# Optimization experiments

Hardware: AMD Instinct MI355X
Metric: run time of the kernel (lower is better)

Reference implementation:

```python
import jax, jax.numpy as jnp
import numpy as np

B, T, N = 16, 2048, 24
K, C_IN, C0, C1 = 3, 1, 64, 64
KS, PRED_LEN = 3, 24
EPS = 1e-5


def _norm_laplacian(adj):
    # L = D^-1/2 A^T D^-1/2 (matches scipy path: (A D^-1/2)^T D^-1/2)
    d = adj.sum(axis=1)
    dis = jnp.where(d > 0, 1.0 / jnp.sqrt(d), 0.0)
    return dis[:, None] * adj.T * dis[None, :]


def _cheb_stack(L, k_terms):
    polys = [jnp.eye(N, dtype=L.dtype), L]
    for _ in range(2, k_terms):
        polys.append(2.0 * L @ polys[-1] - polys[-2])
    return jnp.stack(polys[:k_terms])  # (K, N, N)


def _causal_conv(x, w, b, dilation):
    ks = w.shape[-1]
    pad = (ks - 1) * dilation
    x = jnp.pad(x, ((0, 0), (0, 0), (0, 0), (pad, 0)))
    y = jax.lax.conv_general_dilated(
        x, w, window_strides=(1, 1), padding='VALID',
        rhs_dilation=(1, dilation),
        dimension_numbers=('NCHW', 'OIHW', 'NCHW'))
    return y + b[None, :, None, None]


def _bn(x, g, be):
    # training-mode batch norm over (B, N, T) per channel
    mu = x.mean(axis=(0, 2, 3), keepdims=True)
    var = x.var(axis=(0, 2, 3), keepdims=True)
    return g[None, :, None, None] * (x - mu) * jax.lax.rsqrt(var + EPS) + be[None, :, None, None]


def setup_inputs() -> dict:
    key = jax.random.key(0)
    ks = jax.random.split(key, 16)
    s = 0.05
    return {
        'batch_x': jax.random.normal(ks[0], (B, T, N), jnp.float32),
        'adj': jax.random.uniform(ks[1], (N, N), jnp.float32),
        'theta': jax.random.normal(ks[2], (K, C_IN, C0), jnp.float32),  # Theta per Cheb term
        'w1a': jax.random.normal(ks[3], (C0, C0, 1, KS), jnp.float32) * s,
        'b1a': jnp.zeros((C0,), jnp.float32),
        'g1a': jnp.ones((C0,), jnp.float32), 'be1a': jnp.zeros((C0,), jnp.float32),
        'w1b': jax.random.normal(ks[4], (C0, C0, 1, KS), jnp.float32) * s,
        'b1b': jnp.zeros((C0,), jnp.float32),
        'g1b': jnp.ones((C0,), jnp.float32), 'be1b': jnp.zeros((C0,), jnp.float32),
        'w2a': jax.random.normal(ks[5], (C1, C0, 1, KS), jnp.float32) * s,
        'b2a': jnp.zeros((C1,), jnp.float32),
        'g2a': jnp.ones((C1,), jnp.float32), 'be2a': jnp.zeros((C1,), jnp.float32),
        'w2b': jax.random.normal(ks[6], (C1, C1, 1, KS), jnp.float32) * s,
        'b2b': jnp.zeros((C1,), jnp.float32),
        'g2b': jnp.ones((C1,), jnp.float32), 'be2b': jnp.zeros((C1,), jnp.float32),
        'w_end': jax.random.normal(ks[7], (C1 // 2, C1, 1, 1), jnp.float32) * s,
        'b_end': jnp.zeros((C1 // 2,), jnp.float32),
        'w_end1': jax.random.normal(ks[8], (1, C1 // 2, 1, 2), jnp.float32) * s,
        'b_end1': jnp.zeros((1,), jnp.float32),
    }


def reference(batch_x, adj, theta,
              w1a, b1a, g1a, be1a, w1b, b1b, g1b, be1b,
              w2a, b2a, g2a, be2a, w2b, b2b, g2b, be2b,
              w_end, b_end, w_end1, b_end1):
    # (B, T, N) -> (B, 1, N, T)
    x = jnp.transpose(batch_x, (0, 2, 1))[:, None, :, :]

    # --- Cheb_conv: fused over K terms and all timesteps ---
    L = _norm_laplacian(adj)
    Tk = _cheb_stack(L, K)                       # (K, N, N)
    xp = jnp.transpose(x, (0, 2, 1, 3))          # (B, N, C_in, T)
    # out[b,o,n,t] = sum_{k,m,c} xp[b,m,c,t] Tk[k,m,n] theta[k,c,o]
    gc = jnp.einsum('bmct,kmn,kco->bont', xp, Tk, theta)  # (B, C0, N, T)

    # --- TCN block 1 (dilation 1), residual is identity (C0 == C0) ---
    h = jax.nn.relu(_bn(_causal_conv(gc, w1a, b1a, 1), g1a, be1a))
    h = jax.nn.relu(_bn(_causal_conv(h, w1b, b1b, 1), g1b, be1b))
    out0 = jax.nn.relu(h + gc)

    # --- TCN block 2 (dilation 2), residual identity (C0 == C1), no final relu ---
    h = jax.nn.relu(_bn(_causal_conv(out0, w2a, b2a, 2), g2a, be2a))
    h = jax.nn.relu(_bn(_causal_conv(h, w2b, b2b, 2), g2b, be2b))
    out = h + out0                               # (B, C1, N, T)

    # --- head: 1x1 conv + relu, then (1,2) valid conv -> 1 channel ---
    e = jax.lax.conv_general_dilated(out, w_end, (1, 1), 'VALID',
                                     dimension_numbers=('NCHW', 'OIHW', 'NCHW'))
    e = jax.nn.relu(e + b_end[None, :, None, None])
    e = jax.lax.conv_general_dilated(e, w_end1, (1, 1), 'VALID',
                                     dimension_numbers=('NCHW', 'OIHW', 'NCHW'))
    e = e + b_end1[None, :, None, None]          # (B, 1, N, T-1)
    e = e[:, 0, :, -PRED_LEN:]                   # (B, N, pred_len)
    return jnp.transpose(e, (0, 2, 1))           # (B, pred_len, N)
```

## Files before the change

### kernel.cpp

```cpp
#include <hip/hip_runtime.h>
#include <cmath>

#define TPB 256

typedef __attribute__((ext_vector_type(8)))  short short8;
typedef __attribute__((ext_vector_type(16))) float float16;

static constexpr int  BB   = 16;
static constexpr int  TDIM = 2048;
static constexpr int  NN   = 24;
static constexpr int  P    = BB * NN;
static constexpr int  C    = 64;
static constexpr int  TILE = 256;
static constexpr int  NBT  = TDIM / TILE;
static constexpr int  NSHARD = 64;
static constexpr float INV_CNT = 1.0f / 786432.0f;
static constexpr int  XPITCH = 72;

static constexpr size_t OFF_TK    = 0;
static constexpr size_t OFF_WEFF  = 6912;
static constexpr size_t OFF_WFRAG = 9216;
static constexpr size_t OFF_ST    = 82944;
static constexpr size_t OFF_O0    = 216320;
static constexpr size_t OFF_YT    = 2673920;
static constexpr size_t OFF_S     = 5131520;
static constexpr size_t OFF_YA    = 14568704;
static constexpr size_t OFF_YB    = 115232000;

__device__ __forceinline__ unsigned short f2bf(float f) {
    unsigned int i = __float_as_uint(f);
    i += 0x7FFFu + ((i >> 16) & 1u);
    return (unsigned short)(i >> 16);
}
__device__ __forceinline__ float bf2f(unsigned short u) {
    return __uint_as_float((unsigned)u << 16);
}
__device__ __forceinline__ unsigned pk2bf(float a, float b) {
    unsigned ua = __float_as_uint(a) + 0x8000u;
    unsigned ub = __float_as_uint(b) + 0x8000u;
    return __builtin_amdgcn_perm(ub, ua, 0x07060302u);
}

__device__ __forceinline__
void bn_from_stats(const float* __restrict__ statsIn, const float* __restrict__ g,
                   const float* __restrict__ be, float2* abl, int tid)
{
    const int ch = tid >> 2, q = tid & 3;
    float s1 = 0.f, s2 = 0.f;
    #pragma unroll
    for (int u = 0; u < 4; ++u) {
        float4 a = *(const float4*)(statsIn + tid * 16 + u * 4);
        float4 b = *(const float4*)(statsIn + 4096 + tid * 16 + u * 4);
        s1 += a.x + a.y + a.z + a.w;
        s2 += b.x + b.y + b.z + b.w;
    }
    s1 += __shfl_xor(s1, 1); s1 += __shfl_xor(s1, 2);
    s2 += __shfl_xor(s2, 1); s2 += __shfl_xor(s2, 2);
    if (q == 0) {
        float mu  = s1 * INV_CNT;
        float var = s2 * INV_CNT - mu * mu;
        float a = g[ch] * (1.0f / sqrtf(var + 1e-5f));
        abl[ch] = make_float2(a, be[ch] - mu * a);
    }
}

__global__ __launch_bounds__(TPB)
void prep_kernel(const float* __restrict__ adj, const float* __restrict__ theta,
                 const float* __restrict__ w1a,
                 const float* __restrict__ w1b, const float* __restrict__ w2a,
                 const float* __restrict__ w2b,
                 float* __restrict__ tk, float* __restrict__ weff,
                 unsigned short* __restrict__ wf, float* __restrict__ stats)
{
    const int tid = threadIdx.x;
    if (blockIdx.x < 144) {
        int e = blockIdx.x * TPB + tid;
        int conv = e / 12288, r = e % 12288;
        int oh = r / 6144; r %= 6144;
        int kc = r / 512;  r %= 512;
        int lane = r / 8;
        int jj = r % 8;
        int o = oh * 32 + (lane & 31);
        int K = kc * 16 + (lane >> 5) * 8 + jj;
        int j = K / 64, c2 = K % 64;
        const float* w = (conv == 0) ? w1b : ((conv == 1) ? w2a : w2b);
        wf[e] = f2bf(w[(o * 64 + c2) * 3 + j]);
        return;
    }

    __shared__ float disl[24];
    __shared__ float Ll[576];
    __shared__ float T2l[576];

    for (int e = tid; e < 4 * 8192; e += TPB) stats[e] = 0.f;

    if (tid < 24) {
        float d = 0.f;
        for (int j = 0; j < 24; ++j) d += adj[tid * 24 + j];
        disl[tid] = (d > 0.f) ? 1.0f / sqrtf(d) : 0.f;
    }
    __syncthreads();
    for (int e = tid; e < 576; e += TPB) {
        int i = e / 24, j = e % 24;
        Ll[e] = disl[i] * adj[j * 24 + i] * disl[j];
    }
    __syncthreads();
    for (int e = tid; e < 576; e += TPB) {
        int i = e / 24, j = e % 24;
        float a = 0.f;
        for (int m = 0; m < 24; ++m) a += Ll[i * 24 + m] * Ll[m * 24 + j];
        T2l[e] = 2.f * a - ((i == j) ? 1.f : 0.f);
    }
    __syncthreads();
    for (int e = tid; e < 576; e += TPB) {
        int i = e / 24, j = e % 24;
        tk[e]        = (i == j) ? 1.f : 0.f;
        tk[576 + e]  = Ll[e];
        tk[1152 + e] = T2l[e];
    }
    for (int e = tid; e < 576; e += TPB) {
        int o = e / 9, k = (e % 9) / 3, j = e % 3;
        float a = 0.f;
        for (int c2 = 0; c2 < 64; ++c2)
            a += w1a[(o * 64 + c2) * 3 + j] * theta[k * 64 + c2];
        weff[(k * 3 + j) * 64 + o] = a;
    }
}

__global__ __launch_bounds__(TPB)
void s_kernel(const float* __restrict__ bx, const float* __restrict__ tk,
              float* __restrict__ sbuf)
{
    __shared__ float bxs[256 * 25];
    __shared__ float tkl[576];
    const int tid = threadIdx.x;
    const int blk = blockIdx.x;
    const int b  = blk / 24;
    const int r  = blk % 24;
    const int k  = r >> 3;
    const int t0 = (r & 7) * 256;

    for (int e = tid; e < 576; e += TPB) tkl[e] = tk[k * 576 + e];
    for (int e = tid; e < 256 * 24; e += TPB) {
        int t = e / 24, m = e % 24;
        bxs[t * 25 + m] = bx[((long)b * TDIM + t0 + t) * NN + m];
    }
    __syncthreads();

    const int t = tid;
    float acc[24];
    #pragma unroll
    for (int n = 0; n < 24; ++n) acc[n] = 0.f;
    for (int m = 0; m < 24; ++m) {
        float xb = bxs[t * 25 + m];
        const float* tr = tkl + m * 24;
        #pragma unroll
        for (int n = 0; n < 24; ++n) acc[n] = fmaf(xb, tr[n], acc[n]);
    }
    for (int n = 0; n < 24; ++n)
        sbuf[((long)k * P + b * NN + n) * TDIM + t0 + t] = acc[n];
}

__global__ __launch_bounds__(TPB)
void stats1a_kernel(const float* __restrict__ sbuf, const float* __restrict__ weff,
                    float* __restrict__ statsOut)
{
    __shared__ float4 ssl4[3 * 66];
    __shared__ float4 wl4[144];
    __shared__ float  part[4][2][64];
    const int tid = threadIdx.x;
    const int blk = blockIdx.x;
    const int p  = blk >> 3;
    const int t0 = (blk & 7) * 256;

    for (int e = tid; e < 576; e += TPB) ((float*)wl4)[e] = weff[e];
    for (int e = tid; e < 3 * 65; e += TPB) {
        int k = e / 65, u4 = e % 65;
        int t = t0 - 4 + u4 * 4;
        float4 v = make_float4(0.f, 0.f, 0.f, 0.f);
        if (t >= 0) v = *(const float4*)(sbuf + ((long)k * P + p) * TDIM + t);
        ssl4[k * 66 + u4] = v;
    }
    __syncthreads();

    const int oq = tid & 7;
    const int tq = tid >> 3;
    float acc[8][8];
    #pragma unroll
    for (int i = 0; i < 8; ++i)
        #pragma unroll
        for (int ti = 0; ti < 8; ++ti) acc[i][ti] = 0.f;

    #pragma unroll
    for (int k = 0; k < 3; ++k) {
        float4 x0 = ssl4[k * 66 + tq * 2];
        float4 x1 = ssl4[k * 66 + tq * 2 + 1];
        float4 x2 = ssl4[k * 66 + tq * 2 + 2];
        float xv[12] = { x0.x,x0.y,x0.z,x0.w, x1.x,x1.y,x1.z,x1.w, x2.x,x2.y,x2.z,x2.w };
        #pragma unroll
        for (int j = 0; j < 3; ++j) {
            float4 w0 = wl4[(k * 3 + j) * 16 + oq * 2];
            float4 w1 = wl4[(k * 3 + j) * 16 + oq * 2 + 1];
            float wv[8] = { w0.x,w0.y,w0.z,w0.w, w1.x,w1.y,w1.z,w1.w };
            #pragma unroll
            for (int i = 0; i < 8; ++i)
                #pragma unroll
                for (int ti = 0; ti < 8; ++ti)
                    acc[i][ti] = fmaf(wv[i], xv[ti + 2 + j], acc[i][ti]);
        }
    }

    float s1v[8], s2v[8];
    #pragma unroll
    for (int i = 0; i < 8; ++i) {
        float a1 = 0.f, a2 = 0.f;
        #pragma unroll
        for (int ti = 0; ti < 8; ++ti) { a1 += acc[i][ti]; a2 += acc[i][ti] * acc[i][ti]; }
        s1v[i] = a1; s2v[i] = a2;
    }
    #pragma unroll
    for (int m = 8; m < 64; m <<= 1) {
        #pragma unroll
        for (int i = 0; i < 8; ++i) {
            s1v[i] += __shfl_xor(s1v[i], m);
            s2v[i] += __shfl_xor(s2v[i], m);
        }
    }
    const int wave = tid >> 6, lane = tid & 63;
    if (lane < 8) {
        #pragma unroll
        for (int i = 0; i < 8; ++i) {
            part[wave][0][oq * 8 + i] = s1v[i];
            part[wave][1][oq * 8 + i] = s2v[i];
        }
    }
    __syncthreads();
    if (tid < 128) {
        int s = tid >> 6, o = tid & 63;
        float tot = part[0][s][o] + part[1][s][o] + part[2][s][o] + part[3][s][o];
        atomicAdd(&statsOut[(s * 64 + o) * NSHARD + (blk & 63)], tot);
    }
}

template<int MODE>
__global__ __launch_bounds__(TPB)
void conv_mfma(const float* __restrict__ sbuf, const unsigned short* __restrict__ yin,
               unsigned short* __restrict__ yout, float* __restrict__ ytail,
               const unsigned short* __restrict__ wf, const float* __restrict__ weff,
               const float* __restrict__ statsIn, const float* __restrict__ g,
               const float* __restrict__ be, float* __restrict__ statsOut,
               const float* __restrict__ theta, float* __restrict__ o0s)
{
    __shared__ unsigned short Xl[260 * XPITCH];
    __shared__ float  ssl[(MODE <= 1) ? 3 * 264 : 4];
    __shared__ float  weffl[(MODE == 0) ? 576 : 4];
    __shared__ float  thl[(MODE == 1) ? 192 : 4];
    __shared__ float2 abl[64];
    __shared__ float  parts[(MODE <= 1) ? 4 * 8 * 8 * 2 : 4 * 2 * 16 * 2];

    const int tid  = threadIdx.x;
    const int lane = tid & 63;
    const int w    = tid >> 6;
    const int oh   = w & 1;
    const int l31  = lane & 31;
    const int h    = lane >> 5;
    const int blk  = blockIdx.x;
    const int p    = blk >> 3;
    const int tile = blk & 7;
    const int t0   = tile * TILE;

    short8 af[12];
    #pragma unroll
    for (int kc = 0; kc < 12; ++kc)
        af[kc] = *((const short8*)wf + (oh * 12 + kc) * 64 + lane);

    bn_from_stats(statsIn, g, be, abl, tid);

    if (MODE == 0)
        for (int e = tid; e < 576; e += TPB) weffl[e] = weff[e];
    if (MODE == 1)
        for (int e = tid; e < 192; e += TPB) thl[e] = theta[e];
    if (MODE <= 1) {
        for (int e = tid; e < 3 * 66; e += TPB) {
            int k = e / 66, u4 = e % 66;
            int t = t0 - 8 + u4 * 4;
            float4 v = make_float4(0.f, 0.f, 0.f, 0.f);
            if (t >= 0) v = *(const float4*)(sbuf + ((long)k * P + p) * TDIM + t);
            *(float4*)(ssl + k * 264 + u4 * 4) = v;
        }
    }
    __syncthreads();

    const unsigned short* yinb = (MODE >= 1)
        ? (yin + ((long)p * TDIM + t0 - 4) * 64) : nullptr;
    for (int e = tid; e < 260 * 8; e += TPB) {
        const int tt = e >> 3, cb = e & 7;
        const int t = t0 - 4 + tt;
        float xv[8];
        if (t < 0) {
            #pragma unroll
            for (int r = 0; r < 8; ++r) xv[r] = 0.f;
        } else if (MODE == 0) {
            float sv[9];
            #pragma unroll
            for (int k = 0; k < 3; ++k)
                #pragma unroll
                for (int j = 0; j < 3; ++j)
                    sv[k * 3 + j] = ssl[k * 264 + tt + 2 + j];
            #pragma unroll
            for (int r = 0; r < 8; ++r) {
                int c = cb * 8 + r;
                float raw = 0.f;
                #pragma unroll
                for (int q = 0; q < 9; ++q)
                    raw = fmaf(weffl[q * 64 + c], sv[q], raw);
                float2 ab = abl[c];
                xv[r] = fmaxf(fmaf(ab.x, raw, ab.y), 0.f);
            }
        } else {
            short8 yv8 = *(const short8*)(yinb + (long)e * 8);
            float gcb[3];
            if (MODE == 1) {
                gcb[0] = ssl[      tt + 4];
                gcb[1] = ssl[264 + tt + 4];
                gcb[2] = ssl[528 + tt + 4];
            }
            #pragma unroll
            for (int r = 0; r < 8; ++r) {
                int c = cb * 8 + r;
                float2 ab = abl[c];
                float v = bf2f((unsigned short)yv8[r]);
                float hh = fmaxf(fmaf(ab.x, v, ab.y), 0.f);
                if (MODE == 1) {
                    float gc = thl[c] * gcb[0] + thl[64 + c] * gcb[1] + thl[128 + c] * gcb[2];
                    hh = fmaxf(hh + gc, 0.f);
                }
                xv[r] = hh;
            }
        }
        if (MODE == 1 && tile == 7 && tt >= 235) {
            #pragma unroll
            for (int r = 0; r < 8; ++r)
                o0s[(long)p * 1600 + (cb * 8 + r) * 25 + (tt - 235)] = xv[r];
        }
        uint4 pk;
        pk.x = pk2bf(xv[0], xv[1]);
        pk.y = pk2bf(xv[2], xv[3]);
        pk.z = pk2bf(xv[4], xv[5]);
        pk.w = pk2bf(xv[6], xv[7]);
        *(uint4*)(Xl + tt * XPITCH + cb * 8) = pk;
    }
    __syncthreads();

    float16 acc[4];
    #pragma unroll
    for (int i = 0; i < 4; ++i)
        #pragma unroll
        for (int r = 0; r < 16; ++r) acc[i][r] = 0.f;

    const int tqb = (w >> 1) * 4;
    #pragma unroll
    for (int kc = 0; kc < 12; ++kc) {
        const int j = kc >> 2;
        const int roff = (MODE == 0) ? (2 + j) : (2 * j);
        const int cbase = (kc & 3) * 16 + h * 8;
        #pragma unroll
        for (int i = 0; i < 4; ++i) {
            int row = (tqb + i) * 32 + l31 + roff;
            short8 bfr = *(const short8*)(Xl + row * XPITCH + cbase);
            acc[i] = __builtin_amdgcn_mfma_f32_32x32x16_bf16(af[kc], bfr, acc[i], 0, 0, 0);
        }
    }

    if (MODE <= 1) {
        __syncthreads();

        #pragma unroll
        for (int i = 0; i < 4; ++i) {
            int tl = (tqb + i) * 32 + l31;
            #pragma unroll
            for (int q = 0; q < 4; ++q) {
                int ob = oh * 32 + 8 * q + 4 * h;
                uint2 pk;
                pk.x = pk2bf(acc[i][4 * q + 0], acc[i][4 * q + 1]);
                pk.y = pk2bf(acc[i][4 * q + 2], acc[i][4 * q + 3]);
                *(uint2*)(Xl + tl * XPITCH + ob) = pk;
            }
        }
        __syncthreads();

        const int cb = tid & 7;
        unsigned short* youtb = yout + ((long)p * TDIM + t0) * 64;
        float s1[8], s2[8];
        #pragma unroll
        for (int r = 0; r < 8; ++r) { s1[r] = 0.f; s2[r] = 0.f; }
        for (int e = tid; e < 2048; e += TPB) {
            int tt = e >> 3;
            uint4 v = *(const uint4*)(Xl + tt * XPITCH + cb * 8);
            *(uint4*)(youtb + (long)e * 8) = v;
            unsigned uu[4] = { v.x, v.y, v.z, v.w };
            #pragma unroll
            for (int q = 0; q < 4; ++q) {
                float f0 = __uint_as_float(uu[q] << 16);
                float f1 = __uint_as_float(uu[q] & 0xFFFF0000u);
                s1[2 * q]     += f0;  s2[2 * q]     = fmaf(f0, f0, s2[2 * q]);
                s1[2 * q + 1] += f1;  s2[2 * q + 1] = fmaf(f1, f1, s2[2 * q + 1]);
            }
        }
        #pragma unroll
        for (int m = 8; m <= 32; m <<= 1) {
            #pragma unroll
            for (int r = 0; r < 8; ++r) {
                s1[r] += __shfl_xor(s1[r], m);
                s2[r] += __shfl_xor(s2[r], m);
            }
        }
        if (lane < 8) {
            #pragma unroll
            for (int r = 0; r < 8; ++r) {
                parts[((w * 8 + lane) * 8 + r) * 2 + 0] = s1[r];
                parts[((w * 8 + lane) * 8 + r) * 2 + 1] = s2[r];
            }
        }
        __syncthreads();
        if (tid < 64) {
            int o = tid, cbo = o >> 3, r = o & 7;
            float t1 = 0.f, t2 = 0.f;
            #pragma unroll
            for (int ww = 0; ww < 4; ++ww) {
                t1 += parts[((ww * 8 + cbo) * 8 + r) * 2 + 0];
                t2 += parts[((ww * 8 + cbo) * 8 + r) * 2 + 1];
            }
            atomicAdd(&statsOut[o * NSHARD + (blk & 63)], t1);
            atomicAdd(&statsOut[(64 + o) * NSHARD + (blk & 63)], t2);
        }
    } else {
        if (tile == 7) {
            #pragma unroll
            for (int i = 0; i < 4; ++i) {
                int tg = t0 + (tqb + i) * 32 + l31;
                if (tg >= TDIM - 25) {
                    #pragma unroll
                    for (int r = 0; r < 16; ++r) {
                        int o = oh * 32 + (r & 3) + 8 * (r >> 2) + 4 * h;
                        ytail[((long)p * C + o) * 25 + (tg - (TDIM - 25))] = acc[i][r];
                    }
                }
            }
        }
        float s1[16], s2[16];
        #pragma unroll
        for (int r = 0; r < 16; ++r) {
            float a1 = 0.f, a2 = 0.f;
            #pragma unroll
            for (int i = 0; i < 4; ++i) { float v = acc[i][r]; a1 += v; a2 = fmaf(v, v, a2); }
            s1[r] = a1; s2[r] = a2;
        }
        #pragma unroll
        for (int m = 1; m <= 16; m <<= 1) {
            #pragma unroll
            for (int r = 0; r < 16; ++r) {
                s1[r] += __shfl_xor(s1[r], m);
                s2[r] += __shfl_xor(s2[r], m);
            }
        }
        if (l31 == 0) {
            #pragma unroll
            for (int r = 0; r < 16; ++r) {
                parts[(((w * 2 + h) * 16) + r) * 2 + 0] = s1[r];
                parts[(((w * 2 + h) * 16) + r) * 2 + 1] = s2[r];
            }
        }
        __syncthreads();
        if (tid < 64) {
            int o = tid;
            int ohh = o >> 5, v = o & 31;
            int hh = (v >> 2) & 1, r = (v & 3) + 4 * (v >> 3);
            float t1 = parts[(((ohh * 2 + hh) * 16) + r) * 2 + 0]
                     + parts[((((ohh + 2) * 2 + hh) * 16) + r) * 2 + 0];
            float t2 = parts[(((ohh * 2 + hh) * 16) + r) * 2 + 1]
                     + parts[((((ohh + 2) * 2 + hh) * 16) + r) * 2 + 1];
            atomicAdd(&statsOut[o * NSHARD + (blk & 63)], t1);
            atomicAdd(&statsOut[(64 + o) * NSHARD + (blk & 63)], t2);
        }
    }
}

__global__ __launch_bounds__(TPB)
void end_kernel(const float* __restrict__ ytail, const float* __restrict__ o0s,
                const float* __restrict__ statsIn, const float* __restrict__ g,
                const float* __restrict__ be, const float* __restrict__ w_end,
                const float* __restrict__ b_end, const float* __restrict__ w_end1,
                const float* __restrict__ b_end1, float* __restrict__ out)
{
    __shared__ float2 abl[64];
    __shared__ float outl[64 * 25];
    __shared__ float e1l[32 * 25];
    __shared__ float wendl[2048];
    const int tid = threadIdx.x;
    const int p = blockIdx.x;
    const int b = p / 24, n = p % 24;

    bn_from_stats(statsIn, g, be, abl, tid);
    for (int e = tid; e < 2048; e += TPB) wendl[e] = w_end[e];
    __syncthreads();

    for (int e = tid; e < 1600; e += TPB) {
        int c = e / 25, tau = e % 25;
        float v = ytail[((long)p * C + c) * 25 + tau];
        float2 ab = abl[c];
        outl[e] = fmaxf(ab.x * v + ab.y, 0.f) + o0s[(long)p * 1600 + e];
    }
    __syncthreads();
    for (int e = tid; e < 800; e += TPB) {
        int q = e / 25, tau = e % 25;
        float a = b_end[q];
        for (int c = 0; c < 64; ++c)
            a = fmaf(wendl[q * 64 + c], outl[c * 25 + tau], a);
        e1l[e] = fmaxf(a, 0.f);
    }
    __syncthreads();
    if (tid < 24) {
        float a = b_end1[0];
        #pragma unroll
        for (int q = 0; q < 32; ++q)
            a += w_end1[q * 2] * e1l[q * 25 + tid] + w_end1[q * 2 + 1] * e1l[q * 25 + tid + 1];
        out[((long)b * 24 + tid) * 24 + n] = a;
    }
}

extern "C" void kernel_launch(void* const* d_in, const int* in_sizes, int n_in,
                              void* d_out, int out_size, void* d_ws, size_t ws_size,
                              hipStream_t stream)
{
    (void)in_sizes; (void)n_in; (void)out_size; (void)ws_size;
    const float* bx    = (const float*)d_in[0];
    const float* adj   = (const float*)d_in[1];
    const float* theta = (const float*)d_in[2];
    const float* w1a   = (const float*)d_in[3];
    const float* g1a   = (const float*)d_in[5];
    const float* be1a  = (const float*)d_in[6];
    const float* w1b   = (const float*)d_in[7];
    const float* g1b   = (const float*)d_in[9];
    const float* be1b  = (const float*)d_in[10];
    const float* w2a   = (const float*)d_in[11];
    const float* g2a   = (const float*)d_in[13];
    const float* be2a  = (const float*)d_in[14];
    const float* w2b   = (const float*)d_in[15];
    const float* g2b   = (const float*)d_in[17];
    const float* be2b  = (const float*)d_in[18];
    const float* wend  = (const float*)d_in[19];
    const float* bend  = (const float*)d_in[20];
    const float* wend1 = (const float*)d_in[21];
    const float* bend1 = (const float*)d_in[22];

    char* ws = (char*)d_ws;
    float*          tk    = (float*)(ws + OFF_TK);
    float*          weff  = (float*)(ws + OFF_WEFF);
    unsigned short* wf    = (unsigned short*)(ws + OFF_WFRAG);
    float*          stats = (float*)(ws + OFF_ST);
    float*          o0s   = (float*)(ws + OFF_O0);
    float*          ytail = (float*)(ws + OFF_YT);
    float*          sb    = (float*)(ws + OFF_S);
    unsigned short* yA    = (unsigned short*)(ws + OFF_YA);
    unsigned short* yB    = (unsigned short*)(ws + OFF_YB);

    prep_kernel   <<<145, TPB, 0, stream>>>(adj, theta, w1a, w1b, w2a, w2b,
                                            tk, weff, wf, stats);
    s_kernel      <<<384, TPB, 0, stream>>>(bx, tk, sb);
    stats1a_kernel<<<P * NBT, TPB, 0, stream>>>(sb, weff, stats);

    conv_mfma<0><<<P * NBT, TPB, 0, stream>>>(
        sb, nullptr, yA, nullptr, wf, weff,
        stats, g1a, be1a, stats + 8192, nullptr, nullptr);
    conv_mfma<1><<<P * NBT, TPB, 0, stream>>>(
        sb, yA, yB, nullptr, wf + 12288, nullptr,
        stats + 8192, g1b, be1b, stats + 16384, theta, o0s);
    conv_mfma<2><<<P * NBT, TPB, 0, stream>>>(
        sb, yB, nullptr, ytail, wf + 24576, nullptr,
        stats + 16384, g2a, be2a, stats + 24576, nullptr, nullptr);

    end_kernel<<<P, TPB, 0, stream>>>(ytail, o0s, stats + 24576, g2b, be2b,
                                      wend, bend, wend1, bend1, (float*)d_out);
}
```

Before: 363.1 us.

## Process two nodes per conv block to amortize weight/BN setup and batch loads

Each conv_mfma block now handles two (batch,node) rows, one after the other, so the grid is halved. The weight fragments, BN coefficients and small tables are loaded once and reused for both rows. The per-row input loads are unrolled into a register batch of 9 short8 loads issued before any conversion, which exposes memory-level parallelism. This costs more shared memory for the source staging buffer, fewer blocks in flight, and extra serialization between the two rows through the added syncs.

Result: slower. 447.1 us (+23.1%).

```diff
diff --git a/kernel.cpp b/kernel.cpp
--- a/kernel.cpp
+++ b/kernel.cpp
@@ -10,6 +10,7 @@
 static constexpr int  TDIM = 2048;
 static constexpr int  NN   = 24;
 static constexpr int  P    = BB * NN;
+static constexpr int  HP   = P / 2;
 static constexpr int  C    = 64;
 static constexpr int  TILE = 256;
 static constexpr int  NBT  = TDIM / TILE;
@@ -252,11 +253,11 @@
                const float* __restrict__ theta, float* __restrict__ o0s)
 {
     __shared__ unsigned short Xl[260 * XPITCH];
-    __shared__ float  ssl[(MODE <= 1) ? 3 * 264 : 4];
+    __shared__ float  ssl[(MODE <= 1) ? 2 * 3 * 264 : 4];
     __shared__ float  weffl[(MODE == 0) ? 576 : 4];
     __shared__ float  thl[(MODE == 1) ? 192 : 4];
     __shared__ float2 abl[64];
-    __shared__ float  parts[(MODE <= 1) ? 4 * 8 * 8 * 2 : 4 * 2 * 16 * 2];
+    __shared__ float  parts[(MODE <= 1) ? 512 : 256];
 
     const int tid  = threadIdx.x;
     const int lane = tid & 63;
@@ -265,7 +266,7 @@
     const int l31  = lane & 31;
     const int h    = lane >> 5;
     const int blk  = blockIdx.x;
-    const int p    = blk >> 3;
+    const int pair = blk >> 3;
     const int tile = blk & 7;
     const int t0   = tile * TILE;
 
@@ -276,212 +277,237 @@
 
     bn_from_stats(statsIn, g, be, abl, tid);
 
-    if (MODE == 0)
-        for (int e = tid; e < 576; e += TPB) weffl[e] = weff[e];
-    if (MODE == 1)
-        for (int e = tid; e < 192; e += TPB) thl[e] = theta[e];
+    if (MODE == 0) {
+        #pragma unroll
+        for (int it = 0; it < 3; ++it) {
+            int e = tid + it * 256;
+            if (e < 576) weffl[e] = weff[e];
+        }
+    }
+    if (MODE == 1) {
+        if (tid < 192) thl[tid] = theta[tid];
+    }
     if (MODE <= 1) {
-        for (int e = tid; e < 3 * 66; e += TPB) {
-            int k = e / 66, u4 = e % 66;
-            int t = t0 - 8 + u4 * 4;
-            float4 v = make_float4(0.f, 0.f, 0.f, 0.f);
-            if (t >= 0) v = *(const float4*)(sbuf + ((long)k * P + p) * TDIM + t);
-            *(float4*)(ssl + k * 264 + u4 * 4) = v;
-        }
-    }
-    __syncthreads();
-
-    const unsigned short* yinb = (MODE >= 1)
-        ? (yin + ((long)p * TDIM + t0 - 4) * 64) : nullptr;
-    for (int e = tid; e < 260 * 8; e += TPB) {
-        const int tt = e >> 3, cb = e & 7;
-        const int t = t0 - 4 + tt;
-        float xv[8];
-        if (t < 0) {
-            #pragma unroll
-            for (int r = 0; r < 8; ++r) xv[r] = 0.f;
-        } else if (MODE == 0) {
-            float sv[9];
-            #pragma unroll
-            for (int k = 0; k < 3; ++k)
-                #pragma unroll
-                for (int j = 0; j < 3; ++j)
-                    sv[k * 3 + j] = ssl[k * 264 + tt + 2 + j];
-            #pragma unroll
-            for (int r = 0; r < 8; ++r) {
-                int c = cb * 8 + r;
-                float raw = 0.f;
-                #pragma unroll
-                for (int q = 0; q < 9; ++q)
-                    raw = fmaf(weffl[q * 64 + c], sv[q], raw);
-                float2 ab = abl[c];
-                xv[r] = fmaxf(fmaf(ab.x, raw, ab.y), 0.f);
+        #pragma unroll
+        for (int it = 0; it < 2; ++it) {
+            int e = tid + it * 256;
+            if (e < 396) {
+                int q = e / 198, rr = e % 198;
+                int k = rr / 66, u4 = rr % 66;
+                int t = t0 - 8 + u4 * 4;
+                int pq = pair + q * HP;
+                float4 v = make_float4(0.f, 0.f, 0.f, 0.f);
+                if (t >= 0) v = *(const float4*)(sbuf + ((long)k * P + pq) * TDIM + t);
+                *(float4*)(ssl + q * 792 + k * 264 + u4 * 4) = v;
+            }
+        }
+    }
+
+    for (int q = 0; q < 2; ++q) {
+        const int pp = pair + q * HP;
+        __syncthreads();
+
+        short8 yv[9];
+        if (MODE >= 1) {
+            const unsigned short* yinb = yin + ((long)pp * TDIM + t0 - 4) * 64;
+            #pragma unroll
+            for (int it = 0; it < 9; ++it) {
+                int e = tid + it * 256;
+                int ec = (e < 2080) ? e : 2079;
+                yv[it] = *(const short8*)(yinb + (long)ec * 8);
+            }
+        }
+
+        #pragma unroll
+        for (int it = 0; it < 9; ++it) {
+            const int e = tid + it * 256;
+            if (e >= 2080) break;
+            const int tt = e >> 3, cb = e & 7;
+            const int t = t0 - 4 + tt;
+            float xv[8];
+            if (t < 0) {
+                #pragma unroll
+                for (int r = 0; r < 8; ++r) xv[r] = 0.f;
+            } else if (MODE == 0) {
+                float sv[9];
+                #pragma unroll
+                for (int k = 0; k < 3; ++k)
+                    #pragma unroll
+                    for (int j = 0; j < 3; ++j)
+                        sv[k * 3 + j] = ssl[q * 792 + k * 264 + tt + 2 + j];
+                #pragma unroll
+                for (int r = 0; r < 8; ++r) {
+                    int c = cb * 8 + r;
+                    float raw = 0.f;
+                    #pragma unroll
+                    for (int u = 0; u < 9; ++u)
+                        raw = fmaf(weffl[u * 64 + c], sv[u], raw);
+                    float2 ab = abl[c];
+                    xv[r] = fmaxf(fmaf(ab.x, raw, ab.y), 0.f);
+                }
+            } else {
+                float gcb[3];
+                if (MODE == 1) {
+                    gcb[0] = ssl[q * 792 +       tt + 4];
+                    gcb[1] = ssl[q * 792 + 264 + tt + 4];
+                    gcb[2] = ssl[q * 792 + 528 + tt + 4];
+                }
+                #pragma unroll
+                for (int r = 0; r < 8; ++r) {
+                    int c = cb * 8 + r;
+                    float2 ab = abl[c];
+                    float v = bf2f((unsigned short)yv[it][r]);
+                    float hh = fmaxf(fmaf(ab.x, v, ab.y), 0.f);
+                    if (MODE == 1) {
+                        float gc = thl[c] * gcb[0] + thl[64 + c] * gcb[1] + thl[128 + c] * gcb[2];
+                        hh = fmaxf(hh + gc, 0.f);
+                    }
+                    xv[r] = hh;
+                }
+            }
+            if (MODE == 1 && tile == 7 && tt >= 235) {
+                #pragma unroll
+                for (int r = 0; r < 8; ++r)
+                    o0s[(long)pp * 1600 + (cb * 8 + r) * 25 + (tt - 235)] = xv[r];
+            }
+            uint4 pk;
+            pk.x = pk2bf(xv[0], xv[1]);
+            pk.y = pk2bf(xv[2], xv[3]);
+            pk.z = pk2bf(xv[4], xv[5]);
+            pk.w = pk2bf(xv[6], xv[7]);
+            *(uint4*)(Xl + tt * XPITCH + cb * 8) = pk;
+        }
+        __syncthreads();
+
+        float16 acc[4];
+        #pragma unroll
+        for (int i = 0; i < 4; ++i)
+            #pragma unroll
+            for (int r = 0; r < 16; ++r) acc[i][r] = 0.f;
+
+        const int tqb = (w >> 1) * 4;
+        #pragma unroll
+        for (int kc = 0; kc < 12; ++kc) {
+            const int j = kc >> 2;
+            const int roff = (MODE == 0) ? (2 + j) : (2 * j);
+            const int cbase = (kc & 3) * 16 + h * 8;
+            #pragma unroll
+            for (int i = 0; i < 4; ++i) {
+                int row = (tqb + i) * 32 + l31 + roff;
+                short8 bfr = *(const short8*)(Xl + row * XPITCH + cbase);
+                acc[i] = __builtin_amdgcn_mfma_f32_32x32x16_bf16(af[kc], bfr, acc[i], 0, 0, 0);
+            }
+        }
+
+        if (MODE <= 1) {
+            __syncthreads();
+
+            #pragma unroll
+            for (int i = 0; i < 4; ++i) {
+                int tl = (tqb + i) * 32 + l31;
+                #pragma unroll
+                for (int qq = 0; qq < 4; ++qq) {
+                    int ob = oh * 32 + 8 * qq + 4 * h;
+                    uint2 pk;
+                    pk.x = pk2bf(acc[i][4 * qq + 0], acc[i][4 * qq + 1]);
+                    pk.y = pk2bf(acc[i][4 * qq + 2], acc[i][4 * qq + 3]);
+                    *(uint2*)(Xl + tl * XPITCH + ob) = pk;
+                }
+            }
+            __syncthreads();
+
+            const int cb = tid & 7;
+            unsigned short* youtb = yout + ((long)pp * TDIM + t0) * 64;
+            float s1[8], s2[8];
+            #pragma unroll
+            for (int r = 0; r < 8; ++r) { s1[r] = 0.f; s2[r] = 0.f; }
+            #pragma unroll
+            for (int it = 0; it < 8; ++it) {
+                int e = tid + it * 256;
+                int tt = e >> 3;
+                uint4 v = *(const uint4*)(Xl + tt * XPITCH + cb * 8);
+                *(uint4*)(youtb + (long)e * 8) = v;
+                unsigned uu[4] = { v.x, v.y, v.z, v.w };
+                #pragma unroll
+                for (int qq = 0; qq < 4; ++qq) {
+                    float f0 = __uint_as_float(uu[qq] << 16);
+                    float f1 = __uint_as_float(uu[qq] & 0xFFFF0000u);
+                    s1[2 * qq]     += f0;  s2[2 * qq]     = fmaf(f0, f0, s2[2 * qq]);
+                    s1[2 * qq + 1] += f1;  s2[2 * qq + 1] = fmaf(f1, f1, s2[2 * qq + 1]);
+                }
+            }
+            #pragma unroll
+            for (int m = 8; m <= 32; m <<= 1) {
+                #pragma unroll
+                for (int r = 0; r < 8; ++r) {
+                    s1[r] += __shfl_xor(s1[r], m);
+                    s2[r] += __shfl_xor(s2[r], m);
+                }
+            }
+            if (lane < 8) {
+                float* pw = parts + (w * 8 + lane) * 16;
+                #pragma unroll
+                for (int r = 0; r < 8; ++r) { pw[r * 2] = s1[r]; pw[r * 2 + 1] = s2[r]; }
+            }
+            __syncthreads();
+            if (tid < 64) {
+                int o = tid, cbo = o >> 3, r = o & 7;
+                float t1 = 0.f, t2 = 0.f;
+                #pragma unroll
+                for (int ww = 0; ww < 4; ++ww) {
+                    t1 += parts[(ww * 8 + cbo) * 16 + r * 2];
+                    t2 += parts[(ww * 8 + cbo) * 16 + r * 2 + 1];
+                }
+                atomicAdd(&statsOut[o * NSHARD + (blk & 63)], t1);
+                atomicAdd(&statsOut[(64 + o) * NSHARD + (blk & 63)], t2);
             }
         } else {
-            short8 yv8 = *(const short8*)(yinb + (long)e * 8);
-            float gcb[3];
-            if (MODE == 1) {
-                gcb[0] = ssl[      tt + 4];
-                gcb[1] = ssl[264 + tt + 4];
-                gcb[2] = ssl[528 + tt + 4];
-            }
-            #pragma unroll
-            for (int r = 0; r < 8; ++r) {
-                int c = cb * 8 + r;
-                float2 ab = abl[c];
-                float v = bf2f((unsigned short)yv8[r]);
-                float hh = fmaxf(fmaf(ab.x, v, ab.y), 0.f);
-                if (MODE == 1) {
-                    float gc = thl[c] * gcb[0] + thl[64 + c] * gcb[1] + thl[128 + c] * gcb[2];
-                    hh = fmaxf(hh + gc, 0.f);
-                }
-                xv[r] = hh;
-            }
-        }
-        if (MODE == 1 && tile == 7 && tt >= 235) {
-            #pragma unroll
-            for (int r = 0; r < 8; ++r)
-                o0s[(long)p * 1600 + (cb * 8 + r) * 25 + (tt - 235)] = xv[r];
-        }
-        uint4 pk;
-        pk.x = pk2bf(xv[0], xv[1]);
-        pk.y = pk2bf(xv[2], xv[3]);
-        pk.z = pk2bf(xv[4], xv[5]);
-        pk.w = pk2bf(xv[6], xv[7]);
-        *(uint4*)(Xl + tt * XPITCH + cb * 8) = pk;
-    }
-    __syncthreads();
-
-    float16 acc[4];
-    #pragma unroll
-    for (int i = 0; i < 4; ++i)
-        #pragma unroll
-        for (int r = 0; r < 16; ++r) acc[i][r] = 0.f;
-
-    const int tqb = (w >> 1) * 4;
-    #pragma unroll
-    for (int kc = 0; kc < 12; ++kc) {
-        const int j = kc >> 2;
-        const int roff = (MODE == 0) ? (2 + j) : (2 * j);
-        const int cbase = (kc & 3) * 16 + h * 8;
-        #pragma unroll
-        for (int i = 0; i < 4; ++i) {
-            int row = (tqb + i) * 32 + l31 + roff;
-            short8 bfr = *(const short8*)(Xl + row * XPITCH + cbase);
-            acc[i] = __builtin_amdgcn_mfma_f32_32x32x16_bf16(af[kc], bfr, acc[i], 0, 0, 0);
-        }
-    }
-
-    if (MODE <= 1) {
-        __syncthreads();
-
-        #pragma unroll
-        for (int i = 0; i < 4; ++i) {
-            int tl = (tqb + i) * 32 + l31;
-            #pragma unroll
-            for (int q = 0; q < 4; ++q) {
-                int ob = oh * 32 + 8 * q + 4 * h;
-                uint2 pk;
-                pk.x = pk2bf(acc[i][4 * q + 0], acc[i][4 * q + 1]);
-                pk.y = pk2bf(acc[i][4 * q + 2], acc[i][4 * q + 3]);
-                *(uint2*)(Xl + tl * XPITCH + ob) = pk;
-            }
-        }
-        __syncthreads();
-
-        const int cb = tid & 7;
-        unsigned short* youtb = yout + ((long)p * TDIM + t0) * 64;
-        float s1[8], s2[8];
-        #pragma unroll
-        for (int r = 0; r < 8; ++r) { s1[r] = 0.f; s2[r] = 0.f; }
-        for (int e = tid; e < 2048; e += TPB) {
-            int tt = e >> 3;
-            uint4 v = *(const uint4*)(Xl + tt * XPITCH + cb * 8);
-            *(uint4*)(youtb + (long)e * 8) = v;
-            unsigned uu[4] = { v.x, v.y, v.z, v.w };
-            #pragma unroll
-            for (int q = 0; q < 4; ++q) {
-                float f0 = __uint_as_float(uu[q] << 16);
-                float f1 = __uint_as_float(uu[q] & 0xFFFF0000u);
-                s1[2 * q]     += f0;  s2[2 * q]     = fmaf(f0, f0, s2[2 * q]);
-                s1[2 * q + 1] += f1;  s2[2 * q + 1] = fmaf(f1, f1, s2[2 * q + 1]);
-            }
-        }
-        #pragma unroll
-        for (int m = 8; m <= 32; m <<= 1) {
-            #pragma unroll
-            for (int r = 0; r < 8; ++r) {
-                s1[r] += __shfl_xor(s1[r], m);
-                s2[r] += __shfl_xor(s2[r], m);
-            }
-        }
-        if (lane < 8) {
-            #pragma unroll
-            for (int r = 0; r < 8; ++r) {
-                parts[((w * 8 + lane) * 8 + r) * 2 + 0] = s1[r];
-                parts[((w * 8 + lane) * 8 + r) * 2 + 1] = s2[r];
-            }
-        }
-        __syncthreads();
-        if (tid < 64) {
-            int o = tid, cbo = o >> 3, r = o & 7;
-            float t1 = 0.f, t2 = 0.f;
-            #pragma unroll
-            for (int ww = 0; ww < 4; ++ww) {
-                t1 += parts[((ww * 8 + cbo) * 8 + r) * 2 + 0];
-                t2 += parts[((ww * 8 + cbo) * 8 + r) * 2 + 1];
-            }
-            atomicAdd(&statsOut[o * NSHARD + (blk & 63)], t1);
-            atomicAdd(&statsOut[(64 + o) * NSHARD + (blk & 63)], t2);
-        }
-    } else {
-        if (tile == 7) {
-            #pragma unroll
-            for (int i = 0; i < 4; ++i) {
-                int tg = t0 + (tqb + i) * 32 + l31;
-                if (tg >= TDIM - 25) {
-                    #pragma unroll
-                    for (int r = 0; r < 16; ++r) {
-                        int o = oh * 32 + (r & 3) + 8 * (r >> 2) + 4 * h;
-                        ytail[((long)p * C + o) * 25 + (tg - (TDIM - 25))] = acc[i][r];
+            if (tile == 7) {
+                #pragma unroll
+                for (int i = 0; i < 4; ++i) {
+                    int tg = t0 + (tqb + i) * 32 + l31;
+                    if (tg >= TDIM - 25) {
+                        #pragma unroll
+                        for (int r = 0; r < 16; ++r) {
+                            int o = oh * 32 + (r & 3) + 8 * (r >> 2) + 4 * h;
+                            ytail[((long)pp * C + o) * 25 + (tg - (TDIM - 25))] = acc[i][r];
+                        }
                     }
                 }
             }
-        }
-        float s1[16], s2[16];
-        #pragma unroll
-        for (int r = 0; r < 16; ++r) {
-            float a1 = 0.f, a2 = 0.f;
-            #pragma unroll
-            for (int i = 0; i < 4; ++i) { float v = acc[i][r]; a1 += v; a2 = fmaf(v, v, a2); }
-            s1[r] = a1; s2[r] = a2;
-        }
-        #pragma unroll
-        for (int m = 1; m <= 16; m <<= 1) {
+            float s1[16], s2[16];
             #pragma unroll
             for (int r = 0; r < 16; ++r) {
-                s1[r] += __shfl_xor(s1[r], m);
-                s2[r] += __shfl_xor(s2[r], m);
-            }
-        }
-        if (l31 == 0) {
-            #pragma unroll
-            for (int r = 0; r < 16; ++r) {
-                parts[(((w * 2 + h) * 16) + r) * 2 + 0] = s1[r];
-                parts[(((w * 2 + h) * 16) + r) * 2 + 1] = s2[r];
-            }
-        }
-        __syncthreads();
-        if (tid < 64) {
-            int o = tid;
-            int ohh = o >> 5, v = o & 31;
-            int hh = (v >> 2) & 1, r = (v & 3) + 4 * (v >> 3);
-            float t1 = parts[(((ohh * 2 + hh) * 16) + r) * 2 + 0]
-                     + parts[((((ohh + 2) * 2 + hh) * 16) + r) * 2 + 0];
-            float t2 = parts[(((ohh * 2 + hh) * 16) + r) * 2 + 1]
-                     + parts[((((ohh + 2) * 2 + hh) * 16) + r) * 2 + 1];
-            atomicAdd(&statsOut[o * NSHARD + (blk & 63)], t1);
-            atomicAdd(&statsOut[(64 + o) * NSHARD + (blk & 63)], t2);
+                float a1 = 0.f, a2 = 0.f;
+                #pragma unroll
+                for (int i = 0; i < 4; ++i) { float v = acc[i][r]; a1 += v; a2 = fmaf(v, v, a2); }
+                s1[r] = a1; s2[r] = a2;
+            }
+            #pragma unroll
+            for (int m = 1; m <= 16; m <<= 1) {
+                #pragma unroll
+                for (int r = 0; r < 16; ++r) {
+                    s1[r] += __shfl_xor(s1[r], m);
+                    s2[r] += __shfl_xor(s2[r], m);
+                }
+            }
+            if (l31 == 0) {
+                float* pw = parts + (w * 2 + h) * 32;
+                #pragma unroll
+                for (int r = 0; r < 16; ++r) { pw[r * 2] = s1[r]; pw[r * 2 + 1] = s2[r]; }
+            }
+            __syncthreads();
+            if (tid < 64) {
+                int o = tid;
+                int ohh = o >> 5, v = o & 31;
+                int hh = (v >> 2) & 1, r = (v & 3) + 4 * (v >> 3);
+                float t1 = parts[(ohh * 2 + hh) * 32 + r * 2]
+                         + parts[((ohh + 2) * 2 + hh) * 32 + r * 2];
+                float t2 = parts[(ohh * 2 + hh) * 32 + r * 2 + 1]
+                         + parts[((ohh + 2) * 2 + hh) * 32 + r * 2 + 1];
+                atomicAdd(&statsOut[o * NSHARD + (blk & 63)], t1);
+                atomicAdd(&statsOut[(64 + o) * NSHARD + (blk & 63)], t2);
+            }
         }
     }
 }
@@ -570,13 +596,13 @@
     s_kernel      <<<384, TPB, 0, stream>>>(bx, tk, sb);
     stats1a_kernel<<<P * NBT, TPB, 0, stream>>>(sb, weff, stats);
 
-    conv_mfma<0><<<P * NBT, TPB, 0, stream>>>(
+    conv_mfma<0><<<HP * NBT, TPB, 0, stream>>>(
         sb, nullptr, yA, nullptr, wf, weff,
         stats, g1a, be1a, stats + 8192, nullptr, nullptr);
-    conv_mfma<1><<<P * NBT, TPB, 0, stream>>>(
+    conv_mfma<1><<<HP * NBT, TPB, 0, stream>>>(
         sb, yA, yB, nullptr, wf + 12288, nullptr,
         stats + 8192, g1b, be1b, stats + 16384, theta, o0s);
-    conv_mfma<2><<<P * NBT, TPB, 0, stream>>>(
+    conv_mfma<2><<<HP * NBT, TPB, 0, stream>>>(
         sb, yB, nullptr, ytail, wf + 24576, nullptr,
         stats + 16384, g2a, be2a, stats + 24576, nullptr, nullptr);
 
```

## Precompute BN affine in tiny kernels, swizzle LDS tile, shrink shared memory

Applied to the files above, without the earlier changes.

Moves batch-norm stat reduction out of every conv block into single-block bnprep kernels, so each conv block just loads 64 precomputed scale/shift pairs. Replaces the padded LDS pitch with an XOR-swizzled 64-wide layout and aliases the scratch buffers, cutting shared memory per block. Adds launch_bounds occupancy hint of 4 blocks. Risks extra launch overhead from the four additional kernels.

After: 334.3 us. -7.9%, faster.

```diff
diff --git a/kernel.cpp b/kernel.cpp
--- a/kernel.cpp
+++ b/kernel.cpp
@@ -15,12 +15,12 @@
 static constexpr int  NBT  = TDIM / TILE;
 static constexpr int  NSHARD = 64;
 static constexpr float INV_CNT = 1.0f / 786432.0f;
-static constexpr int  XPITCH = 72;
 
 static constexpr size_t OFF_TK    = 0;
 static constexpr size_t OFF_WEFF  = 6912;
 static constexpr size_t OFF_WFRAG = 9216;
 static constexpr size_t OFF_ST    = 82944;
+static constexpr size_t OFF_BNAB  = 214016;
 static constexpr size_t OFF_O0    = 216320;
 static constexpr size_t OFF_YT    = 2673920;
 static constexpr size_t OFF_S     = 5131520;
@@ -40,28 +40,8 @@
     unsigned ub = __float_as_uint(b) + 0x8000u;
     return __builtin_amdgcn_perm(ub, ua, 0x07060302u);
 }
-
-__device__ __forceinline__
-void bn_from_stats(const float* __restrict__ statsIn, const float* __restrict__ g,
-                   const float* __restrict__ be, float2* abl, int tid)
-{
-    const int ch = tid >> 2, q = tid & 3;
-    float s1 = 0.f, s2 = 0.f;
-    #pragma unroll
-    for (int u = 0; u < 4; ++u) {
-        float4 a = *(const float4*)(statsIn + tid * 16 + u * 4);
-        float4 b = *(const float4*)(statsIn + 4096 + tid * 16 + u * 4);
-        s1 += a.x + a.y + a.z + a.w;
-        s2 += b.x + b.y + b.z + b.w;
-    }
-    s1 += __shfl_xor(s1, 1); s1 += __shfl_xor(s1, 2);
-    s2 += __shfl_xor(s2, 1); s2 += __shfl_xor(s2, 2);
-    if (q == 0) {
-        float mu  = s1 * INV_CNT;
-        float var = s2 * INV_CNT - mu * mu;
-        float a = g[ch] * (1.0f / sqrtf(var + 1e-5f));
-        abl[ch] = make_float2(a, be[ch] - mu * a);
-    }
+__device__ __forceinline__ int xidx(int tt, int ci) {
+    return tt * 64 + (((ci ^ (tt & 7)) << 3));
 }
 
 __global__ __launch_bounds__(TPB)
@@ -128,6 +108,29 @@
 }
 
 __global__ __launch_bounds__(TPB)
+void bnprep_kernel(const float* __restrict__ stats, const float* __restrict__ g,
+                   const float* __restrict__ be, float2* __restrict__ ab)
+{
+    const int tid = threadIdx.x;
+    const int ch = tid >> 2, q = tid & 3;
+    float s1 = 0.f, s2 = 0.f;
+    #pragma unroll
+    for (int u = 0; u < 16; ++u) {
+        int sh = q * 16 + u;
+        s1 += stats[ch * 64 + sh];
+        s2 += stats[(64 + ch) * 64 + sh];
+    }
+    s1 += __shfl_xor(s1, 1); s1 += __shfl_xor(s1, 2);
+    s2 += __shfl_xor(s2, 1); s2 += __shfl_xor(s2, 2);
+    if (q == 0) {
+        float mu  = s1 * INV_CNT;
+        float var = s2 * INV_CNT - mu * mu;
+        float a = g[ch] * (1.0f / sqrtf(var + 1e-5f));
+        ab[ch] = make_float2(a, be[ch] - mu * a);
+    }
+}
+
+__global__ __launch_bounds__(TPB)
 void s_kernel(const float* __restrict__ bx, const float* __restrict__ tk,
               float* __restrict__ sbuf)
 {
@@ -243,20 +246,22 @@
 }
 
 template<int MODE>
-__global__ __launch_bounds__(TPB)
+__global__ __launch_bounds__(TPB, 4)
 void conv_mfma(const float* __restrict__ sbuf, const unsigned short* __restrict__ yin,
                unsigned short* __restrict__ yout, float* __restrict__ ytail,
                const unsigned short* __restrict__ wf, const float* __restrict__ weff,
-               const float* __restrict__ statsIn, const float* __restrict__ g,
-               const float* __restrict__ be, float* __restrict__ statsOut,
+               const float2* __restrict__ bnab, float* __restrict__ statsOut,
                const float* __restrict__ theta, float* __restrict__ o0s)
 {
-    __shared__ unsigned short Xl[260 * XPITCH];
-    __shared__ float  ssl[(MODE <= 1) ? 3 * 264 : 4];
-    __shared__ float  weffl[(MODE == 0) ? 576 : 4];
-    __shared__ float  thl[(MODE == 1) ? 192 : 4];
+    constexpr int SCR = (MODE == 0) ? (792 + 576) : ((MODE == 1) ? (792 + 192) : 512);
+    __shared__ unsigned short Xl[260 * 64];
+    __shared__ float  scratch[SCR];
     __shared__ float2 abl[64];
-    __shared__ float  parts[(MODE <= 1) ? 4 * 8 * 8 * 2 : 4 * 2 * 16 * 2];
+
+    float* const ssl   = scratch;
+    float* const weffl = scratch + 792;
+    float* const thl   = scratch + 792;
+    float* const parts = scratch;
 
     const int tid  = threadIdx.x;
     const int lane = tid & 63;
@@ -274,12 +279,11 @@
     for (int kc = 0; kc < 12; ++kc)
         af[kc] = *((const short8*)wf + (oh * 12 + kc) * 64 + lane);
 
-    bn_from_stats(statsIn, g, be, abl, tid);
-
+    if (tid < 64) abl[tid] = bnab[tid];
     if (MODE == 0)
         for (int e = tid; e < 576; e += TPB) weffl[e] = weff[e];
     if (MODE == 1)
-        for (int e = tid; e < 192; e += TPB) thl[e] = theta[e];
+        if (tid < 192) thl[tid] = theta[tid];
     if (MODE <= 1) {
         for (int e = tid; e < 3 * 66; e += TPB) {
             int k = e / 66, u4 = e % 66;
@@ -312,8 +316,8 @@
                 int c = cb * 8 + r;
                 float raw = 0.f;
                 #pragma unroll
-                for (int q = 0; q < 9; ++q)
-                    raw = fmaf(weffl[q * 64 + c], sv[q], raw);
+                for (int u = 0; u < 9; ++u)
+                    raw = fmaf(weffl[u * 64 + c], sv[u], raw);
                 float2 ab = abl[c];
                 xv[r] = fmaxf(fmaf(ab.x, raw, ab.y), 0.f);
             }
@@ -348,7 +352,7 @@
         pk.y = pk2bf(xv[2], xv[3]);
         pk.z = pk2bf(xv[4], xv[5]);
         pk.w = pk2bf(xv[6], xv[7]);
-        *(uint4*)(Xl + tt * XPITCH + cb * 8) = pk;
+        *(uint4*)(Xl + xidx(tt, cb)) = pk;
     }
     __syncthreads();
 
@@ -363,11 +367,11 @@
     for (int kc = 0; kc < 12; ++kc) {
         const int j = kc >> 2;
         const int roff = (MODE == 0) ? (2 + j) : (2 * j);
-        const int cbase = (kc & 3) * 16 + h * 8;
+        const int ci = (kc & 3) * 2 + h;
         #pragma unroll
         for (int i = 0; i < 4; ++i) {
             int row = (tqb + i) * 32 + l31 + roff;
-            short8 bfr = *(const short8*)(Xl + row * XPITCH + cbase);
+            short8 bfr = *(const short8*)(Xl + xidx(row, ci));
             acc[i] = __builtin_amdgcn_mfma_f32_32x32x16_bf16(af[kc], bfr, acc[i], 0, 0, 0);
         }
     }
@@ -379,12 +383,12 @@
         for (int i = 0; i < 4; ++i) {
             int tl = (tqb + i) * 32 + l31;
             #pragma unroll
-            for (int q = 0; q < 4; ++q) {
-                int ob = oh * 32 + 8 * q + 4 * h;
+            for (int qq = 0; qq < 4; ++qq) {
+                int ci = oh * 4 + qq;
                 uint2 pk;
-                pk.x = pk2bf(acc[i][4 * q + 0], acc[i][4 * q + 1]);
-                pk.y = pk2bf(acc[i][4 * q + 2], acc[i][4 * q + 3]);
-                *(uint2*)(Xl + tl * XPITCH + ob) = pk;
+                pk.x = pk2bf(acc[i][4 * qq + 0], acc[i][4 * qq + 1]);
+                pk.y = pk2bf(acc[i][4 * qq + 2], acc[i][4 * qq + 3]);
+                *(uint2*)(Xl + xidx(tl, ci) + 4 * h) = pk;
             }
         }
         __syncthreads();
@@ -396,15 +400,15 @@
         for (int r = 0; r < 8; ++r) { s1[r] = 0.f; s2[r] = 0.f; }
         for (int e = tid; e < 2048; e += TPB) {
             int tt = e >> 3;
-            uint4 v = *(const uint4*)(Xl + tt * XPITCH + cb * 8);
+            uint4 v = *(const uint4*)(Xl + xidx(tt, cb));
             *(uint4*)(youtb + (long)e * 8) = v;
             unsigned uu[4] = { v.x, v.y, v.z, v.w };
             #pragma unroll
-            for (int q = 0; q < 4; ++q) {
-                float f0 = __uint_as_float(uu[q] << 16);
-                float f1 = __uint_as_float(uu[q] & 0xFFFF0000u);
-                s1[2 * q]     += f0;  s2[2 * q]     = fmaf(f0, f0, s2[2 * q]);
-                s1[2 * q + 1] += f1;  s2[2 * q + 1] = fmaf(f1, f1, s2[2 * q + 1]);
+            for (int qq = 0; qq < 4; ++qq) {
+                float f0 = __uint_as_float(uu[qq] << 16);
+                float f1 = __uint_as_float(uu[qq] & 0xFFFF0000u);
+                s1[2 * qq]     += f0;  s2[2 * qq]     = fmaf(f0, f0, s2[2 * qq]);
+                s1[2 * qq + 1] += f1;  s2[2 * qq + 1] = fmaf(f1, f1, s2[2 * qq + 1]);
             }
         }
         #pragma unroll
@@ -416,11 +420,9 @@
             }
         }
         if (lane < 8) {
-            #pragma unroll
-            for (int r = 0; r < 8; ++r) {
-                parts[((w * 8 + lane) * 8 + r) * 2 + 0] = s1[r];
-                parts[((w * 8 + lane) * 8 + r) * 2 + 1] = s2[r];
-            }
+            float* pw = parts + (w * 8 + lane) * 16;
+            #pragma unroll
+            for (int r = 0; r < 8; ++r) { pw[r * 2] = s1[r]; pw[r * 2 + 1] = s2[r]; }
         }
         __syncthreads();
         if (tid < 64) {
@@ -428,8 +430,8 @@
             float t1 = 0.f, t2 = 0.f;
             #pragma unroll
             for (int ww = 0; ww < 4; ++ww) {
-                t1 += parts[((ww * 8 + cbo) * 8 + r) * 2 + 0];
-                t2 += parts[((ww * 8 + cbo) * 8 + r) * 2 + 1];
+                t1 += parts[(ww * 8 + cbo) * 16 + r * 2];
+                t2 += parts[(ww * 8 + cbo) * 16 + r * 2 + 1];
             }
             atomicAdd(&statsOut[o * NSHARD + (blk & 63)], t1);
             atomicAdd(&statsOut[(64 + o) * NSHARD + (blk & 63)], t2);
@@ -465,21 +467,19 @@
             }
         }
         if (l31 == 0) {
-            #pragma unroll
-            for (int r = 0; r < 16; ++r) {
-                parts[(((w * 2 + h) * 16) + r) * 2 + 0] = s1[r];
-                parts[(((w * 2 + h) * 16) + r) * 2 + 1] = s2[r];
-            }
+            float* pw = parts + (w * 2 + h) * 32;
+            #pragma unroll
+            for (int r = 0; r < 16; ++r) { pw[r * 2] = s1[r]; pw[r * 2 + 1] = s2[r]; }
         }
         __syncthreads();
         if (tid < 64) {
             int o = tid;
             int ohh = o >> 5, v = o & 31;
             int hh = (v >> 2) & 1, r = (v & 3) + 4 * (v >> 3);
-            float t1 = parts[(((ohh * 2 + hh) * 16) + r) * 2 + 0]
-                     + parts[((((ohh + 2) * 2 + hh) * 16) + r) * 2 + 0];
-            float t2 = parts[(((ohh * 2 + hh) * 16) + r) * 2 + 1]
-                     + parts[((((ohh + 2) * 2 + hh) * 16) + r) * 2 + 1];
+            float t1 = parts[(ohh * 2 + hh) * 32 + r * 2]
+                     + parts[((ohh + 2) * 2 + hh) * 32 + r * 2];
+            float t2 = parts[(ohh * 2 + hh) * 32 + r * 2 + 1]
+                     + parts[((ohh + 2) * 2 + hh) * 32 + r * 2 + 1];
             atomicAdd(&statsOut[o * NSHARD + (blk & 63)], t1);
             atomicAdd(&statsOut[(64 + o) * NSHARD + (blk & 63)], t2);
         }
@@ -488,8 +488,7 @@
 
 __global__ __launch_bounds__(TPB)
 void end_kernel(const float* __restrict__ ytail, const float* __restrict__ o0s,
-                const float* __restrict__ statsIn, const float* __restrict__ g,
-                const float* __restrict__ be, const float* __restrict__ w_end,
+                const float2* __restrict__ bnab, const float* __restrict__ w_end,
                 const float* __restrict__ b_end, const float* __restrict__ w_end1,
                 const float* __restrict__ b_end1, float* __restrict__ out)
 {
@@ -501,7 +500,7 @@
     const int p = blockIdx.x;
     const int b = p / 24, n = p % 24;
 
-    bn_from_stats(statsIn, g, be, abl, tid);
+    if (tid < 64) abl[tid] = bnab[tid];
     for (int e = tid; e < 2048; e += TPB) wendl[e] = w_end[e];
     __syncthreads();
 
@@ -559,6 +558,7 @@
     float*          weff  = (float*)(ws + OFF_WEFF);
     unsigned short* wf    = (unsigned short*)(ws + OFF_WFRAG);
     float*          stats = (float*)(ws + OFF_ST);
+    float2*         bnab  = (float2*)(ws + OFF_BNAB);
     float*          o0s   = (float*)(ws + OFF_O0);
     float*          ytail = (float*)(ws + OFF_YT);
     float*          sb    = (float*)(ws + OFF_S);
@@ -569,17 +569,23 @@
                                             tk, weff, wf, stats);
     s_kernel      <<<384, TPB, 0, stream>>>(bx, tk, sb);
     stats1a_kernel<<<P * NBT, TPB, 0, stream>>>(sb, weff, stats);
+    bnprep_kernel <<<1, TPB, 0, stream>>>(stats,         g1a, be1a, bnab);
 
     conv_mfma<0><<<P * NBT, TPB, 0, stream>>>(
         sb, nullptr, yA, nullptr, wf, weff,
-        stats, g1a, be1a, stats + 8192, nullptr, nullptr);
+        bnab, stats + 8192, nullptr, nullptr);
+    bnprep_kernel <<<1, TPB, 0, stream>>>(stats + 8192,  g1b, be1b, bnab + 64);
+
     conv_mfma<1><<<P * NBT, TPB, 0, stream>>>(
         sb, yA, yB, nullptr, wf + 12288, nullptr,
-        stats + 8192, g1b, be1b, stats + 16384, theta, o0s);
+        bnab + 64, stats + 16384, theta, o0s);
+    bnprep_kernel <<<1, TPB, 0, stream>>>(stats + 16384, g2a, be2a, bnab + 128);
+
     conv_mfma<2><<<P * NBT, TPB, 0, stream>>>(
         sb, yB, nullptr, ytail, wf + 24576, nullptr,
-        stats + 16384, g2a, be2a, stats + 24576, nullptr, nullptr);
-
-    end_kernel<<<P, TPB, 0, stream>>>(ytail, o0s, stats + 24576, g2b, be2b,
+        bnab + 128, stats + 24576, nullptr, nullptr);
+    bnprep_kernel <<<1, TPB, 0, stream>>>(stats + 24576, g2b, be2b, bnab + 192);
+
+    end_kernel<<<P, TPB, 0, stream>>>(ytail, o0s, bnab + 192,
                                       wend, bend, wend1, bend1, (float*)d_out);
 }
```
